# Kernel tuning notes

Hardware: AMD Instinct MI355X
Metric: run time of the kernel (lower is better)

## Reference

```python
import jax, jax.numpy as jnp
import numpy as np

N_STEPS = 10
DT = 0.01
TAU = 0.1
LAM = 0.1


def setup_inputs() -> dict:
    key = jax.random.key(0)
    k1, k2 = jax.random.split(key)
    x = jax.random.normal(k1, (4, 2048, 1024), dtype=jnp.float32)
    W = jax.random.normal(k2, (1024, 4096), dtype=jnp.float32) * 0.02
    return {"x": x, "W": W}


def reference(x, W):
    orig_shape = x.shape
    D = orig_shape[-1]
    x_flat = x.reshape(-1, D)                      # [N, d_model]
    b = x_flat @ W                                 # [N, d_lca]
    G = W.T @ W                                    # [d_lca, d_lca]
    G = G - jnp.diag(jnp.diag(G))                  # zero self-inhibition
    u0 = jnp.zeros_like(b)

    def step(u, _):
        a = jax.nn.relu(u - LAM)
        du = (b - a @ G - u) / TAU
        return u + DT * du, None

    u, _ = jax.lax.scan(step, u0, None, length=N_STEPS)
    a = jax.nn.relu(u - LAM)
    out = a @ W.T                                  # [N, d_model]
    return out.reshape(orig_shape)
```

## Files before the change

### kernel.cpp

```cpp
#include <hip/hip_runtime.h>
#include <hip/hip_bf16.h>


typedef __bf16 bf16_t;
typedef __bf16 bf16x8 __attribute__((ext_vector_type(8)));
typedef __bf16 bf16x4 __attribute__((ext_vector_type(4)));
typedef float  f32x4  __attribute__((ext_vector_type(4)));

__device__ __forceinline__ void g2lds16(const void* g, void* l) {
    __builtin_amdgcn_global_load_lds(
        (const __attribute__((address_space(1))) void*)g,
        (__attribute__((address_space(3))) void*)l,
        16, 0, 0);
}

enum { MODE_B = 0, MODE_T = 1, MODE_STEP2 = 2, MODE_OUT = 3 };

template<int MODE, int BM>
__global__ __launch_bounds__((BM == 256) ? 512 : 256)
void gemm_bt(const bf16_t* __restrict__ A, const bf16_t* __restrict__ Bt,
             int N, int K,
             float*  __restrict__ outF,
             bf16_t* __restrict__ outH,
             bf16_t* __restrict__ bb,
             bf16_t* __restrict__ u,
             const float* __restrict__ g)
{
    constexpr int NT  = (BM == 256) ? 512 : 256;
    constexpr int RPI = NT / 4;

    __shared__ __attribute__((aligned(16))) bf16_t As[2 * BM * 32];
    __shared__ __attribute__((aligned(16))) bf16_t Bs[2 * 128 * 32];

    const int t  = threadIdx.x;
    const int l  = t & 63;
    const int w  = t >> 6;
    const int wm = (w >> 1) * 64;
    const int wn = (w & 1) * 64;

    const int rowA = blockIdx.y * BM;
    const int colB = blockIdx.x * 128;

    const int srow = t >> 2;
    const int skc  = (t & 3) * 8;
    const bf16_t* gA = A  + (size_t)(rowA + srow) * K + skc;
    const bf16_t* gB = Bt + (size_t)(colB + srow) * K + skc;
    const size_t halfA = (size_t)RPI * K;
    char* lA = (char*)As + t * 16;
    char* lB = (char*)Bs + t * 16;

    f32x4 acc[4][4];
#pragma unroll
    for (int i = 0; i < 4; ++i)
#pragma unroll
        for (int j = 0; j < 4; ++j)
#pragma unroll
            for (int r = 0; r < 4; ++r) acc[i][j][r] = 0.f;

    const int lrow = l & 15;
    const int lk   = (l >> 4) * 8;
    const bf16_t* pA = As + (wm + lrow) * 32 + lk;
    const bf16_t* pB = Bs + (wn + lrow) * 32 + lk;

    for (int k0 = 0; k0 < K; k0 += 64) {
#pragma unroll
        for (int p = 0; p < 2; ++p) {
            const int kp = k0 + p * 32;
            g2lds16(gA + kp,         lA + p * (BM * 64));
            g2lds16(gA + kp + halfA, lA + p * (BM * 64) + RPI * 64);
            if (NT == 512) {
                g2lds16(gB + kp, lB + p * 8192);
            } else {
                g2lds16(gB + kp,                  lB + p * 8192);
                g2lds16(gB + kp + (size_t)64 * K, lB + p * 8192 + 4096);
            }
        }
        __syncthreads();

#pragma unroll
        for (int p = 0; p < 2; ++p) {
            const bf16_t* qA = pA + p * (BM * 32);
            const bf16_t* qB = pB + p * 4096;
            bf16x8 af[4], bfr[4];
#pragma unroll
            for (int i = 0; i < 4; ++i) af[i]  = *(const bf16x8*)(qA + i * 16 * 32);
#pragma unroll
            for (int j = 0; j < 4; ++j) bfr[j] = *(const bf16x8*)(qB + j * 16 * 32);
#pragma unroll
            for (int i = 0; i < 4; ++i)
#pragma unroll
                for (int j = 0; j < 4; ++j)
                    acc[i][j] = __builtin_amdgcn_mfma_f32_16x16x32_bf16(
                        bfr[j], af[i], acc[i][j], 0, 0, 0);
        }
        __syncthreads();
    }

    const int m0 = rowA + wm + (l & 15);
    const int n0 = colB + wn + ((l >> 4) * 4);

    f32x4 gvv[4];
    if (MODE == MODE_STEP2) {
#pragma unroll
        for (int j = 0; j < 4; ++j) gvv[j] = *(const f32x4*)(g + n0 + j * 16);
    }

#pragma unroll
    for (int i = 0; i < 4; ++i) {
        const int m = m0 + i * 16;
#pragma unroll
        for (int j = 0; j < 4; ++j) {
            const size_t idx = (size_t)m * N + (n0 + j * 16);
            const f32x4 c = acc[i][j];
            if (MODE == MODE_T) {
                bf16x4 o;
#pragma unroll
                for (int r = 0; r < 4; ++r) o[r] = (bf16_t)c[r];
                *(bf16x4*)(outH + idx) = o;
            } else if (MODE == MODE_B) {
                bf16x4 ob, ou, oa;
#pragma unroll
                for (int r = 0; r < 4; ++r) {
                    const float un = 0.1f * c[r];
                    ob[r] = (bf16_t)c[r];
                    ou[r] = (bf16_t)un;
                    oa[r] = (bf16_t)fmaxf(un - 0.1f, 0.f);
                }
                *(bf16x4*)(bb   + idx) = ob;
                *(bf16x4*)(u    + idx) = ou;
                *(bf16x4*)(outH + idx) = oa;
            } else if (MODE == MODE_STEP2) {
                const bf16x4 uv = *(const bf16x4*)(u  + idx);
                const bf16x4 bv = *(const bf16x4*)(bb + idx);
                bf16x4 ou, oa;
#pragma unroll
                for (int r = 0; r < 4; ++r) {
                    const float uo = (float)uv[r];
                    const float ao = fmaxf(uo - 0.1f, 0.f);
                    const float un = 0.9f * uo + 0.1f * (float)bv[r]
                                   - 0.1f * c[r] + 0.1f * ao * gvv[j][r];
                    ou[r] = (bf16_t)un;
                    oa[r] = (bf16_t)fmaxf(un - 0.1f, 0.f);
                }
                *(bf16x4*)(u    + idx) = ou;
                *(bf16x4*)(outH + idx) = oa;
            } else {
                *(f32x4*)(outF + idx) = c;
            }
        }
    }
}

__global__ void cast_x_kernel(const float* __restrict__ x, bf16_t* __restrict__ xh, int n) {
    int i = blockIdx.x * 256 + threadIdx.x;
    if (i < n) xh[i] = (bf16_t)x[i];
}

__global__ void prep_w_kernel(const float* __restrict__ W,
                              bf16_t* __restrict__ Wh, bf16_t* __restrict__ WT) {
    int i = blockIdx.x * 256 + threadIdx.x;
    if (i < 1024 * 4096) {
        int k = i >> 12;
        int n = i & 4095;
        bf16_t v = (bf16_t)W[i];
        Wh[i] = v;
        WT[(size_t)n * 1024 + k] = v;
    }
}

__global__ void prep_g_kernel(const float* __restrict__ W, float* __restrict__ g) {
    int j = blockIdx.x * 256 + threadIdx.x;
    if (j < 4096) {
        float s = 0.f;
        for (int k = 0; k < 1024; ++k) {
            float v = W[(size_t)k * 4096 + j];
            s += v * v;
        }
        g[j] = s;
    }
}

extern "C" void kernel_launch(void* const* d_in, const int* in_sizes, int n_in,
                              void* d_out, int out_size, void* d_ws, size_t ws_size,
                              hipStream_t stream)
{
    const float* x = (const float*)d_in[0];
    const float* W = (const float*)d_in[1];

    bf16_t* xh = (bf16_t*)d_out;
    bf16_t* tt = (bf16_t*)d_out;
    float*  gd = (float*)((char*)d_out + 16777216);

    char* ws = (char*)d_ws;
    bf16_t* a  = (bf16_t*)(ws);
    bf16_t* bb = (bf16_t*)(ws + 67108864);
    bf16_t* u  = (bf16_t*)(ws + 134217728);
    bf16_t* Wh = (bf16_t*)(ws + 201326592);
    bf16_t* WT = (bf16_t*)(ws + 209715200);

    cast_x_kernel<<<8388608 / 256, 256, 0, stream>>>(x, xh, 8388608);
    prep_w_kernel<<<4194304 / 256, 256, 0, stream>>>(W, Wh, WT);
    prep_g_kernel<<<16, 256, 0, stream>>>(W, gd);

    gemm_bt<MODE_B, 256><<<dim3(32, 32), 512, 0, stream>>>(xh, WT, 4096, 1024,
                                                           nullptr, a, bb, u, nullptr);
    for (int s = 0; s < 9; ++s) {
        gemm_bt<MODE_T, 128><<<dim3(8, 64), 256, 0, stream>>>(a, Wh, 1024, 4096,
                                                              nullptr, tt, nullptr, nullptr, nullptr);
        gemm_bt<MODE_STEP2, 256><<<dim3(32, 32), 512, 0, stream>>>(tt, WT, 4096, 1024,
                                                                   nullptr, a, bb, u, gd);
    }
    gemm_bt<MODE_OUT, 128><<<dim3(8, 64), 256, 0, stream>>>(a, Wh, 1024, 4096,
                                                            (float*)d_out, nullptr, nullptr, nullptr, nullptr);
}
```

Before: 2.125 ms.

## Double-buffer GEMM LDS with BK=64, swizzled layout, larger tiles and setprio

Reworks the bf16 MFMA GEMM into a two-slot LDS pipeline. The next K-tile is prefetched with global_load_lds while the current one is computed, and fine-grained vmcnt waits plus raw barriers replace the old full __syncthreads. The K tile grows to 64 with an XOR-swizzled LDS layout to avoid bank conflicts, and all variants now use 512 threads with 256x128 or 256x256 block tiles. s_setprio is raised around the MFMA bursts. The aim is to hide global-load latency and raise data reuse, at the cost of more LDS (up to 128KB per block) and more accumulator registers, which lowers occupancy.

```diff
diff --git a/kernel.cpp b/kernel.cpp
--- a/kernel.cpp
+++ b/kernel.cpp
@@ -14,10 +14,16 @@
         16, 0, 0);
 }
 
+template<int N> __device__ __forceinline__ void waitv() {
+    if constexpr (N == 0)      asm volatile("s_waitcnt vmcnt(0)" ::: "memory");
+    else if constexpr (N == 6) asm volatile("s_waitcnt vmcnt(6)" ::: "memory");
+    else if constexpr (N == 8) asm volatile("s_waitcnt vmcnt(8)" ::: "memory");
+}
+
 enum { MODE_B = 0, MODE_T = 1, MODE_STEP2 = 2, MODE_OUT = 3 };
 
-template<int MODE, int BM>
-__global__ __launch_bounds__((BM == 256) ? 512 : 256)
+template<int MODE, int BN>
+__global__ __launch_bounds__(512, 2)
 void gemm_bt(const bf16_t* __restrict__ A, const bf16_t* __restrict__ Bt,
              int N, int K,
              float*  __restrict__ outF,
@@ -26,98 +32,112 @@
              bf16_t* __restrict__ u,
              const float* __restrict__ g)
 {
-    constexpr int NT  = (BM == 256) ? 512 : 256;
-    constexpr int RPI = NT / 4;
-
-    __shared__ __attribute__((aligned(16))) bf16_t As[2 * BM * 32];
-    __shared__ __attribute__((aligned(16))) bf16_t Bs[2 * 128 * 32];
+    constexpr int BM = 256;
+    constexpr int WN_WAVES = (BN == 256) ? 4 : 2;
+    constexpr int WM_WAVES = 8 / WN_WAVES;
+    constexpr int WTM = BM / WM_WAVES;
+    constexpr int WTN = BN / WN_WAVES;
+    constexpr int FM = WTM / 16;
+    constexpr int FN = WTN / 16;
+    constexpr int LPS_A = BM / 64;
+    constexpr int LPS_B = BN / 64;
+    constexpr int LPS = LPS_A + LPS_B;
+
+    __shared__ __attribute__((aligned(16))) bf16_t As[2 * BM * 64];
+    __shared__ __attribute__((aligned(16))) bf16_t Bs[2 * BN * 64];
 
     const int t  = threadIdx.x;
     const int l  = t & 63;
     const int w  = t >> 6;
-    const int wm = (w >> 1) * 64;
-    const int wn = (w & 1) * 64;
+    const int wm = (w / WN_WAVES) * WTM;
+    const int wn = (w % WN_WAVES) * WTN;
 
     const int rowA = blockIdx.y * BM;
-    const int colB = blockIdx.x * 128;
-
-    const int srow = t >> 2;
-    const int skc  = (t & 3) * 8;
-    const bf16_t* gA = A  + (size_t)(rowA + srow) * K + skc;
-    const bf16_t* gB = Bt + (size_t)(colB + srow) * K + skc;
-    const size_t halfA = (size_t)RPI * K;
+    const int colB = blockIdx.x * BN;
+
+    const int srow = t >> 3;
+    const int scol = ((t & 7) * 8) ^ (((t >> 5) & 1) * 16);
+    const bf16_t* gA = A  + (size_t)(rowA + srow) * K + scol;
+    const bf16_t* gB = Bt + (size_t)(colB + srow) * K + scol;
     char* lA = (char*)As + t * 16;
     char* lB = (char*)Bs + t * 16;
 
-    f32x4 acc[4][4];
-#pragma unroll
-    for (int i = 0; i < 4; ++i)
-#pragma unroll
-        for (int j = 0; j < 4; ++j)
+    f32x4 acc[FM][FN];
+#pragma unroll
+    for (int i = 0; i < FM; ++i)
+#pragma unroll
+        for (int j = 0; j < FN; ++j)
 #pragma unroll
             for (int r = 0; r < 4; ++r) acc[i][j][r] = 0.f;
 
-    const int lrow = l & 15;
-    const int lk   = (l >> 4) * 8;
-    const bf16_t* pA = As + (wm + lrow) * 32 + lk;
-    const bf16_t* pB = Bs + (wn + lrow) * 32 + lk;
-
-    for (int k0 = 0; k0 < K; k0 += 64) {
+    const int lrow  = l & 15;
+    const int cfrag = ((l >> 4) * 8) ^ (((l >> 2) & 1) * 16);
+    const bf16_t* pA0 = As + (wm + lrow) * 64 + cfrag;
+    const bf16_t* pB0 = Bs + (wn + lrow) * 64 + cfrag;
+
+    auto STAGE = [&](int kt, int slot) {
+        const int k0 = kt * 64;
+#pragma unroll
+        for (int q = 0; q < LPS_A; ++q)
+            g2lds16(gA + (size_t)(q * 64) * K + k0, lA + slot * (BM * 128) + q * 8192);
+#pragma unroll
+        for (int q = 0; q < LPS_B; ++q)
+            g2lds16(gB + (size_t)(q * 64) * K + k0, lB + slot * (BN * 128) + q * 8192);
+    };
+
+    const int NK = K >> 6;
+    STAGE(0, 0);
+    STAGE(1, 1);
+
+    for (int k = 0; k < NK; ++k) {
+        if (k + 1 < NK) waitv<LPS>(); else waitv<0>();
+        asm volatile("s_barrier" ::: "memory");
+
+        const bf16_t* sA = pA0 + (k & 1) * (BM * 64);
+        const bf16_t* sB = pB0 + (k & 1) * (BN * 64);
 #pragma unroll
         for (int p = 0; p < 2; ++p) {
-            const int kp = k0 + p * 32;
-            g2lds16(gA + kp,         lA + p * (BM * 64));
-            g2lds16(gA + kp + halfA, lA + p * (BM * 64) + RPI * 64);
-            if (NT == 512) {
-                g2lds16(gB + kp, lB + p * 8192);
-            } else {
-                g2lds16(gB + kp,                  lB + p * 8192);
-                g2lds16(gB + kp + (size_t)64 * K, lB + p * 8192 + 4096);
-            }
-        }
-        __syncthreads();
-
-#pragma unroll
-        for (int p = 0; p < 2; ++p) {
-            const bf16_t* qA = pA + p * (BM * 32);
-            const bf16_t* qB = pB + p * 4096;
-            bf16x8 af[4], bfr[4];
-#pragma unroll
-            for (int i = 0; i < 4; ++i) af[i]  = *(const bf16x8*)(qA + i * 16 * 32);
-#pragma unroll
-            for (int j = 0; j < 4; ++j) bfr[j] = *(const bf16x8*)(qB + j * 16 * 32);
-#pragma unroll
-            for (int i = 0; i < 4; ++i)
-#pragma unroll
-                for (int j = 0; j < 4; ++j)
+            bf16x8 af[FM], bfr[FN];
+#pragma unroll
+            for (int i = 0; i < FM; ++i) af[i]  = *(const bf16x8*)(sA + i * 1024 + p * 32);
+#pragma unroll
+            for (int j = 0; j < FN; ++j) bfr[j] = *(const bf16x8*)(sB + j * 1024 + p * 32);
+            __builtin_amdgcn_s_setprio(1);
+#pragma unroll
+            for (int i = 0; i < FM; ++i)
+#pragma unroll
+                for (int j = 0; j < FN; ++j)
                     acc[i][j] = __builtin_amdgcn_mfma_f32_16x16x32_bf16(
                         bfr[j], af[i], acc[i][j], 0, 0, 0);
+            __builtin_amdgcn_s_setprio(0);
         }
-        __syncthreads();
+        asm volatile("s_waitcnt lgkmcnt(0)" ::: "memory");
+        asm volatile("s_barrier" ::: "memory");
+        if (k + 2 < NK) STAGE(k + 2, k & 1);
     }
 
     const int m0 = rowA + wm + (l & 15);
     const int n0 = colB + wn + ((l >> 4) * 4);
 
-    f32x4 gvv[4];
-    if (MODE == MODE_STEP2) {
-#pragma unroll
-        for (int j = 0; j < 4; ++j) gvv[j] = *(const f32x4*)(g + n0 + j * 16);
-    }
-
-#pragma unroll
-    for (int i = 0; i < 4; ++i) {
+    f32x4 gvv[FN];
+    if constexpr (MODE == MODE_STEP2) {
+#pragma unroll
+        for (int j = 0; j < FN; ++j) gvv[j] = *(const f32x4*)(g + n0 + j * 16);
+    }
+
+#pragma unroll
+    for (int i = 0; i < FM; ++i) {
         const int m = m0 + i * 16;
 #pragma unroll
-        for (int j = 0; j < 4; ++j) {
+        for (int j = 0; j < FN; ++j) {
             const size_t idx = (size_t)m * N + (n0 + j * 16);
             const f32x4 c = acc[i][j];
-            if (MODE == MODE_T) {
+            if constexpr (MODE == MODE_T) {
                 bf16x4 o;
 #pragma unroll
                 for (int r = 0; r < 4; ++r) o[r] = (bf16_t)c[r];
                 *(bf16x4*)(outH + idx) = o;
-            } else if (MODE == MODE_B) {
+            } else if constexpr (MODE == MODE_B) {
                 bf16x4 ob, ou, oa;
 #pragma unroll
                 for (int r = 0; r < 4; ++r) {
@@ -129,7 +149,7 @@
                 *(bf16x4*)(bb   + idx) = ob;
                 *(bf16x4*)(u    + idx) = ou;
                 *(bf16x4*)(outH + idx) = oa;
-            } else if (MODE == MODE_STEP2) {
+            } else if constexpr (MODE == MODE_STEP2) {
                 const bf16x4 uv = *(const bf16x4*)(u  + idx);
                 const bf16x4 bv = *(const bf16x4*)(bb + idx);
                 bf16x4 ou, oa;
@@ -202,14 +222,14 @@
     prep_w_kernel<<<4194304 / 256, 256, 0, stream>>>(W, Wh, WT);
     prep_g_kernel<<<16, 256, 0, stream>>>(W, gd);
 
-    gemm_bt<MODE_B, 256><<<dim3(32, 32), 512, 0, stream>>>(xh, WT, 4096, 1024,
+    gemm_bt<MODE_B, 256><<<dim3(16, 32), 512, 0, stream>>>(xh, WT, 4096, 1024,
                                                            nullptr, a, bb, u, nullptr);
     for (int s = 0; s < 9; ++s) {
-        gemm_bt<MODE_T, 128><<<dim3(8, 64), 256, 0, stream>>>(a, Wh, 1024, 4096,
+        gemm_bt<MODE_T, 128><<<dim3(8, 32), 512, 0, stream>>>(a, Wh, 1024, 4096,
                                                               nullptr, tt, nullptr, nullptr, nullptr);
-        gemm_bt<MODE_STEP2, 256><<<dim3(32, 32), 512, 0, stream>>>(tt, WT, 4096, 1024,
+        gemm_bt<MODE_STEP2, 256><<<dim3(16, 32), 512, 0, stream>>>(tt, WT, 4096, 1024,
                                                                    nullptr, a, bb, u, gd);
     }
-    gemm_bt<MODE_OUT, 128><<<dim3(8, 64), 256, 0, stream>>>(a, Wh, 1024, 4096,
+    gemm_bt<MODE_OUT, 128><<<dim3(8, 32), 512, 0, stream>>>(a, Wh, 1024, 4096,
                                                             (float*)d_out, nullptr, nullptr, nullptr, nullptr);
 }
```

Result: slower. 2.257 ms (+6.2%).
